# Kernel optimization log

Hardware: AMD Instinct MI355X
Metric: run time of the kernel (lower is better)

## Reference

```python
import jax, jax.numpy as jnp
import numpy as np

K = 16          # number of nearest neighbors (init kwarg k)
EPS = 1e-3      # denom threshold from the original code


def setup_inputs() -> dict:
    key = jax.random.key(0)
    k1, k2, k3 = jax.random.split(key, 3)
    V, F = 5000, 10000
    vertices = jax.random.normal(k1, (V, 3), dtype=jnp.float32)
    faces = jax.random.randint(k2, (F, 3), 0, V)
    probabilities = jax.random.uniform(k3, (F,), dtype=jnp.float32)
    return {"vertices": vertices, "faces": faces, "probabilities": probabilities}


def reference(vertices, faces, probabilities):
    F = faces.shape[0]
    pos = vertices[faces]                       # [F,3,3] triangle vertex coords
    bary = pos.mean(axis=1)                     # [F,3] barycenters

    # brute-force kNN over barycenters (x == y, so self is included like torch_geometric knn)
    sq = jnp.sum(bary * bary, axis=-1)          # [F]
    d2 = sq[:, None] + sq[None, :] - 2.0 * (bary @ bary.T)   # [F,F]
    _, nbr = jax.lax.top_k(-d2, K)              # [F,K] neighbor face indices

    # face normals
    e1 = pos[:, 1] - pos[:, 0]
    e2 = pos[:, 2] - pos[:, 0]
    n = jnp.cross(e1, e2)
    n = n / jnp.maximum(jnp.linalg.norm(n, axis=-1, keepdims=True), 1e-12)  # [F,3]

    # per (tri, neighbor, triangle-edge) plane intersection test
    nb_pos = pos[nbr]                           # [F,K,3,3] neighbor triangle vertices
    l0 = nb_pos                                 # segment starts
    l1 = jnp.roll(nb_pos, -1, axis=2)           # segment ends (k -> (k+1)%3)
    n_b = n[:, None, None, :]                   # [F,1,1,3]
    p0_b = pos[:, 0][:, None, None, :]          # [F,1,1,3] plane point of tri

    denom = jnp.sum(n_b * (l1 - l0), axis=-1)   # [F,K,3]
    numer = jnp.sum(n_b * (p0_b - l0), axis=-1) # [F,K,3]
    safe_denom = jnp.where(jnp.abs(denom) < EPS, 1.0, denom)
    t = numer / safe_denom
    hit = (jnp.abs(denom) >= EPS) & (t > 0.0) & (t < 1.0)   # [F,K,3]

    # early break in original => at most 1 increment per (tri, neighbor) pair
    pen = jnp.any(hit, axis=-1) & (nbr != jnp.arange(F)[:, None])  # [F,K]

    # scatter-add penetrations into neighbor_idx
    faces_penetrated = jnp.zeros((F,), jnp.float32).at[nbr.ravel()].add(
        pen.ravel().astype(jnp.float32))

    return jnp.dot(probabilities, faces_penetrated) / F
```

## Files before the change

kernel.cpp:

```cpp
#include <hip/hip_runtime.h>
#include <math.h>

#define KNN 16
#define EPS_F 0.001f
#define BLK 256

#define REP16(M) M(0) M(1) M(2) M(3) M(4) M(5) M(6) M(7) \
                 M(8) M(9) M(10) M(11) M(12) M(13) M(14) M(15)

#define CEAI(p,a,b) { int _lo = min(p##a, p##b); int _hi = max(p##a, p##b); p##a = _lo; p##b = _hi; }
#define CEDI(p,a,b) { int _lo = min(p##a, p##b); int _hi = max(p##a, p##b); p##a = _hi; p##b = _lo; }

#define SORT16I(p) \
  CEAI(p,0,1) CEDI(p,2,3) CEAI(p,4,5) CEDI(p,6,7) CEAI(p,8,9) CEDI(p,10,11) CEAI(p,12,13) CEDI(p,14,15) \
  CEAI(p,0,2) CEAI(p,1,3) CEDI(p,4,6) CEDI(p,5,7) CEAI(p,8,10) CEAI(p,9,11) CEDI(p,12,14) CEDI(p,13,15) \
  CEAI(p,0,1) CEAI(p,2,3) CEDI(p,4,5) CEDI(p,6,7) CEAI(p,8,9) CEAI(p,10,11) CEDI(p,12,13) CEDI(p,14,15) \
  CEAI(p,0,4) CEAI(p,1,5) CEAI(p,2,6) CEAI(p,3,7) CEDI(p,8,12) CEDI(p,9,13) CEDI(p,10,14) CEDI(p,11,15) \
  CEAI(p,0,2) CEAI(p,1,3) CEAI(p,4,6) CEAI(p,5,7) CEDI(p,8,10) CEDI(p,9,11) CEDI(p,12,14) CEDI(p,13,15) \
  CEAI(p,0,1) CEAI(p,2,3) CEAI(p,4,5) CEAI(p,6,7) CEDI(p,8,9) CEDI(p,10,11) CEDI(p,12,13) CEDI(p,14,15) \
  CEAI(p,0,8) CEAI(p,1,9) CEAI(p,2,10) CEAI(p,3,11) CEAI(p,4,12) CEAI(p,5,13) CEAI(p,6,14) CEAI(p,7,15) \
  CEAI(p,0,4) CEAI(p,1,5) CEAI(p,2,6) CEAI(p,3,7) CEAI(p,8,12) CEAI(p,9,13) CEAI(p,10,14) CEAI(p,11,15) \
  CEAI(p,0,2) CEAI(p,1,3) CEAI(p,4,6) CEAI(p,5,7) CEAI(p,8,10) CEAI(p,9,11) CEAI(p,12,14) CEAI(p,13,15) \
  CEAI(p,0,1) CEAI(p,2,3) CEAI(p,4,5) CEAI(p,6,7) CEAI(p,8,9) CEAI(p,10,11) CEAI(p,12,13) CEAI(p,14,15)

#define RESORT16I(p) \
  CEAI(p,0,8) CEAI(p,1,9) CEAI(p,2,10) CEAI(p,3,11) CEAI(p,4,12) CEAI(p,5,13) CEAI(p,6,14) CEAI(p,7,15) \
  CEAI(p,0,4) CEAI(p,1,5) CEAI(p,2,6) CEAI(p,3,7) CEAI(p,8,12) CEAI(p,9,13) CEAI(p,10,14) CEAI(p,11,15) \
  CEAI(p,0,2) CEAI(p,1,3) CEAI(p,4,6) CEAI(p,5,7) CEAI(p,8,10) CEAI(p,9,11) CEAI(p,12,14) CEAI(p,13,15) \
  CEAI(p,0,1) CEAI(p,2,3) CEAI(p,4,5) CEAI(p,6,7) CEAI(p,8,9) CEAI(p,10,11) CEAI(p,12,13) CEAI(p,14,15)

#define MERGE16I(r,x) \
  r##0=min(r##0,x##15); r##1=min(r##1,x##14); r##2=min(r##2,x##13); r##3=min(r##3,x##12); \
  r##4=min(r##4,x##11); r##5=min(r##5,x##10); r##6=min(r##6,x##9);  r##7=min(r##7,x##8);  \
  r##8=min(r##8,x##7);  r##9=min(r##9,x##6);  r##10=min(r##10,x##5); r##11=min(r##11,x##4); \
  r##12=min(r##12,x##3); r##13=min(r##13,x##2); r##14=min(r##14,x##1); r##15=min(r##15,x##0); \
  RESORT16I(r)

__device__ __forceinline__ float dist2(float4 q, float4 p) {
    return (q.w + p.w) - 2.0f * (q.x*p.x + q.y*p.y + q.z*p.z);
}

__device__ __forceinline__ int packkey(float d2, int j) {
    return (__float_as_int(d2) & 0xFFFFC000) | j;
}

__global__ __launch_bounds__(BLK) void prep_kernel(
    const float* __restrict__ verts, const int* __restrict__ faces,
    float4* __restrict__ baryq, float* __restrict__ nrm,
    float* __restrict__ p0s, int F)
{
    int f = blockIdx.x * BLK + threadIdx.x;
    if (f >= F) return;
    int i0 = faces[3*f+0], i1 = faces[3*f+1], i2 = faces[3*f+2];
    float ax = verts[3*i0+0], ay = verts[3*i0+1], az = verts[3*i0+2];
    float bx = verts[3*i1+0], by = verts[3*i1+1], bz = verts[3*i1+2];
    float cx = verts[3*i2+0], cy = verts[3*i2+1], cz = verts[3*i2+2];
    float gx = (ax + bx + cx) / 3.0f;
    float gy = (ay + by + cy) / 3.0f;
    float gz = (az + bz + cz) / 3.0f;
    float sq = gx*gx + gy*gy + gz*gz;
    baryq[f] = make_float4(gx, gy, gz, sq);
    float e1x = bx-ax, e1y = by-ay, e1z = bz-az;
    float e2x = cx-ax, e2y = cy-ay, e2z = cz-az;
    float nx = e1y*e2z - e1z*e2y;
    float ny = e1z*e2x - e1x*e2z;
    float nz = e1x*e2y - e1y*e2x;
    float len = sqrtf(nx*nx + ny*ny + nz*nz);
    float dn = fmaxf(len, 1e-12f);
    nrm[3*f+0] = nx/dn; nrm[3*f+1] = ny/dn; nrm[3*f+2] = nz/dn;
    p0s[3*f+0] = ax; p0s[3*f+1] = ay; p0s[3*f+2] = az;
}

__global__ __launch_bounds__(BLK) void knn_keys(
    const float4* __restrict__ baryq, int* __restrict__ cand_k,
    int F, int chunkLen)
{
    __shared__ float4 sb[BLK];
    int tid = threadIdx.x;
    int qi = blockIdx.x * BLK + tid;
    int qc = min(qi, F-1);
    float4 q = baryq[qc];
    #define DECLR(m) int r##m = 0x7fffffff;
    REP16(DECLR)
    #undef DECLR
    int jb = blockIdx.y * chunkLen;
    int je = min(jb + chunkLen, F);
    for (int base = jb; base < je; base += BLK) {
        int j = base + tid;
        sb[tid] = (j < je) ? baryq[j] : make_float4(0.f, 0.f, 0.f, INFINITY);
        __syncthreads();
        #pragma unroll 1
        for (int g = 0; g < BLK; g += 16) {
            #define MKKEY(m) int x##m = packkey(dist2(q, sb[g+(m)]), base+g+(m));
            REP16(MKKEY)
            #undef MKKEY
            SORT16I(x)
            MERGE16I(r, x)
        }
        __syncthreads();
    }
    if (qi < F) {
        size_t cb = (size_t)blockIdx.y * KNN * F + qi;
        #define STR(m) cand_k[cb + (size_t)(m) * F] = r##m;
        REP16(STR)
        #undef STR
    }
}

__global__ __launch_bounds__(BLK) void merge_nbr(
    const int* __restrict__ cand_k, int* __restrict__ nbr, int F, int nchunk)
{
    int qi = blockIdx.x * BLK + threadIdx.x;
    if (qi >= F) return;
    #define LDR(m) int r##m = cand_k[(size_t)(m) * F + qi];
    REP16(LDR)
    #undef LDR
    for (int c = 1; c < nchunk; ++c) {
        size_t cb = (size_t)c * KNN * F + qi;
        #define LDX(m) int x##m = cand_k[cb + (size_t)(m) * F];
        REP16(LDX)
        #undef LDX
        MERGE16I(r, x)
    }
    size_t ob = (size_t)qi * KNN;
    #define STN(m) nbr[ob + (m)] = r##m & 0x3FFF;
    REP16(STN)
    #undef STN
}

__device__ __forceinline__ bool edge_test(
    float nx, float ny, float nz, float px, float py, float pz,
    float ax, float ay, float az, float bx, float by, float bz)
{
    float denom = nx*(bx-ax) + ny*(by-ay) + nz*(bz-az);
    if (fabsf(denom) < EPS_F) return false;
    float numer = nx*(px-ax) + ny*(py-ay) + nz*(pz-az);
    float t = numer / denom;
    return (t > 0.0f) && (t < 1.0f);
}

__global__ __launch_bounds__(BLK) void pen_kernel(
    const float* __restrict__ verts, const int* __restrict__ faces,
    const float* __restrict__ prob, const int* __restrict__ nbr,
    const float* __restrict__ nrm, const float* __restrict__ p0s,
    float* __restrict__ partial, int F)
{
    int t = blockIdx.x * BLK + threadIdx.x;
    float val = 0.0f;
    int total = F * KNN;
    if (t < total) {
        int i = t >> 4;
        int j = nbr[t];
        if (j != i) {
            float nx = nrm[3*i+0], ny = nrm[3*i+1], nz = nrm[3*i+2];
            float px = p0s[3*i+0], py = p0s[3*i+1], pz = p0s[3*i+2];
            int j0 = faces[3*j+0], j1 = faces[3*j+1], j2 = faces[3*j+2];
            float ax = verts[3*j0+0], ay = verts[3*j0+1], az = verts[3*j0+2];
            float bx = verts[3*j1+0], by = verts[3*j1+1], bz = verts[3*j1+2];
            float cx = verts[3*j2+0], cy = verts[3*j2+1], cz = verts[3*j2+2];
            bool hit = edge_test(nx,ny,nz, px,py,pz, ax,ay,az, bx,by,bz)
                    || edge_test(nx,ny,nz, px,py,pz, bx,by,bz, cx,cy,cz)
                    || edge_test(nx,ny,nz, px,py,pz, cx,cy,cz, ax,ay,az);
            if (hit) val = prob[j];
        }
    }
    __shared__ float red[BLK];
    red[threadIdx.x] = val;
    __syncthreads();
    #pragma unroll
    for (int s = BLK/2; s > 0; s >>= 1) {
        if (threadIdx.x < s) red[threadIdx.x] += red[threadIdx.x + s];
        __syncthreads();
    }
    if (threadIdx.x == 0) partial[blockIdx.x] = red[0];
}

__global__ __launch_bounds__(BLK) void final_reduce(
    const float* __restrict__ partial, int n, float* __restrict__ out, int F)
{
    __shared__ float red[BLK];
    float s = 0.0f;
    for (int i = threadIdx.x; i < n; i += BLK) s += partial[i];
    red[threadIdx.x] = s;
    __syncthreads();
    #pragma unroll
    for (int st = BLK/2; st > 0; st >>= 1) {
        if (threadIdx.x < st) red[threadIdx.x] += red[threadIdx.x + st];
        __syncthreads();
    }
    if (threadIdx.x == 0) out[0] = red[0] / (float)F;
}

extern "C" void kernel_launch(void* const* d_in, const int* in_sizes, int n_in,
                              void* d_out, int out_size, void* d_ws, size_t ws_size,
                              hipStream_t stream)
{
    const float* verts = (const float*)d_in[0];
    const int*   faces = (const int*)d_in[1];
    const float* prob  = (const float*)d_in[2];
    float* out = (float*)d_out;
    int F = in_sizes[2];

    size_t off = 0;
    auto carve = [&](size_t bytes) {
        size_t cur = off;
        off += (bytes + 255) & ~(size_t)255;
        return cur;
    };
    char* w = (char*)d_ws;
    int nPenBlocks = (F * KNN + BLK - 1) / BLK;
    float4* baryq  = (float4*)(w + carve((size_t)F * sizeof(float4)));
    float*  nrm    = (float*)(w + carve((size_t)F * 3 * sizeof(float)));
    float*  p0s    = (float*)(w + carve((size_t)F * 3 * sizeof(float)));
    int*    nbr    = (int*)(w + carve((size_t)F * KNN * sizeof(int)));
    float*  partial= (float*)(w + carve((size_t)nPenBlocks * sizeof(float)));

    size_t perChunk = (size_t)F * KNN * sizeof(int) + 512;
    size_t remain = (ws_size > off) ? (ws_size - off) : 0;
    int nchunk = (int)(remain / perChunk);
    if (nchunk > 40) nchunk = 40;
    if (nchunk < 1) nchunk = 1;
    int chunkLen = (F + nchunk - 1) / nchunk;
    chunkLen = ((chunkLen + BLK - 1) / BLK) * BLK;
    nchunk = (F + chunkLen - 1) / chunkLen;
    int* cand_k = (int*)(w + carve((size_t)F * KNN * nchunk * sizeof(int)));

    int qBlocks = (F + BLK - 1) / BLK;

    prep_kernel<<<qBlocks, BLK, 0, stream>>>(verts, faces, baryq, nrm, p0s, F);
    knn_keys<<<dim3(qBlocks, nchunk), BLK, 0, stream>>>(baryq, cand_k, F, chunkLen);
    merge_nbr<<<qBlocks, BLK, 0, stream>>>(cand_k, nbr, F, nchunk);
    pen_kernel<<<nPenBlocks, BLK, 0, stream>>>(
        verts, faces, prob, nbr, nrm, p0s, partial, F);
    final_reduce<<<1, BLK, 0, stream>>>(partial, nPenBlocks, out, F);
}
```

Measured before the change: 96.36 us.

## Process two queries per thread in kNN and split candidate merge into two stages

The kNN kernel now runs 128-thread blocks where each thread keeps two query points and two top-16 lists. Each shared-memory candidate load is reused for both queries, and the inner loop is bounded by the valid chunk length so chunks can be 16-aligned instead of 256-aligned. The serial merge over up to 40 chunks becomes a two-level merge: groups of 8 chunks are merged in parallel across a 2D grid, then the groups are merged in a final pass. The goal is less shared-memory traffic per distance, finer chunk splitting, and more parallel merging. The cost is roughly double the register use per thread, which can lower occupancy, plus an extra kernel launch and intermediate buffer.

```diff
diff --git a/kernel.cpp b/kernel.cpp
--- a/kernel.cpp
+++ b/kernel.cpp
@@ -4,6 +4,7 @@
 #define KNN 16
 #define EPS_F 0.001f
 #define BLK 256
+#define BLKK 128
 
 #define REP16(M) M(0) M(1) M(2) M(3) M(4) M(5) M(6) M(7) \
                  M(8) M(9) M(10) M(11) M(12) M(13) M(14) M(15)
@@ -71,53 +72,87 @@
     p0s[3*f+0] = ax; p0s[3*f+1] = ay; p0s[3*f+2] = az;
 }
 
-__global__ __launch_bounds__(BLK) void knn_keys(
+__global__ __launch_bounds__(BLKK) void knn_keys(
     const float4* __restrict__ baryq, int* __restrict__ cand_k,
     int F, int chunkLen)
 {
-    __shared__ float4 sb[BLK];
+    __shared__ float4 sb[BLKK];
     int tid = threadIdx.x;
-    int qi = blockIdx.x * BLK + tid;
-    int qc = min(qi, F-1);
-    float4 q = baryq[qc];
-    #define DECLR(m) int r##m = 0x7fffffff;
-    REP16(DECLR)
-    #undef DECLR
+    int qa = blockIdx.x * (2*BLKK) + tid;
+    int qb = qa + BLKK;
+    float4 qA = baryq[min(qa, F-1)];
+    float4 qB = baryq[min(qb, F-1)];
+    #define DECLAB(m) int a##m = 0x7fffffff; int b##m = 0x7fffffff;
+    REP16(DECLAB)
+    #undef DECLAB
     int jb = blockIdx.y * chunkLen;
     int je = min(jb + chunkLen, F);
-    for (int base = jb; base < je; base += BLK) {
+    for (int base = jb; base < je; base += BLKK) {
         int j = base + tid;
         sb[tid] = (j < je) ? baryq[j] : make_float4(0.f, 0.f, 0.f, INFINITY);
         __syncthreads();
+        int lim = min(BLKK, je - base);
         #pragma unroll 1
-        for (int g = 0; g < BLK; g += 16) {
-            #define MKKEY(m) int x##m = packkey(dist2(q, sb[g+(m)]), base+g+(m));
-            REP16(MKKEY)
-            #undef MKKEY
-            SORT16I(x)
-            MERGE16I(r, x)
+        for (int g = 0; g < lim; g += 16) {
+            #define MKK(m) int xA##m, xB##m; { float4 P = sb[g+(m)]; \
+                int cj = base + g + (m); \
+                xA##m = packkey(dist2(qA, P), cj); \
+                xB##m = packkey(dist2(qB, P), cj); }
+            REP16(MKK)
+            #undef MKK
+            SORT16I(xA) SORT16I(xB)
+            MERGE16I(a, xA) MERGE16I(b, xB)
         }
         __syncthreads();
     }
-    if (qi < F) {
-        size_t cb = (size_t)blockIdx.y * KNN * F + qi;
-        #define STR(m) cand_k[cb + (size_t)(m) * F] = r##m;
-        REP16(STR)
-        #undef STR
-    }
-}
-
-__global__ __launch_bounds__(BLK) void merge_nbr(
-    const int* __restrict__ cand_k, int* __restrict__ nbr, int F, int nchunk)
+    size_t cb = (size_t)blockIdx.y * KNN * F;
+    if (qa < F) {
+        #define STA(m) cand_k[cb + (size_t)(m) * F + qa] = a##m;
+        REP16(STA)
+        #undef STA
+    }
+    if (qb < F) {
+        #define STB(m) cand_k[cb + (size_t)(m) * F + qb] = b##m;
+        REP16(STB)
+        #undef STB
+    }
+}
+
+__global__ __launch_bounds__(BLK) void merge_stage1(
+    const int* __restrict__ cand_k, int* __restrict__ cand2, int F, int nchunk)
 {
     int qi = blockIdx.x * BLK + threadIdx.x;
     if (qi >= F) return;
-    #define LDR(m) int r##m = cand_k[(size_t)(m) * F + qi];
+    int g = blockIdx.y;
+    int c0 = g * 8, c1 = min(c0 + 8, nchunk);
+    size_t b0 = (size_t)c0 * KNN * F + qi;
+    #define LDR(m) int r##m = cand_k[b0 + (size_t)(m) * F];
     REP16(LDR)
     #undef LDR
-    for (int c = 1; c < nchunk; ++c) {
+    for (int c = c0 + 1; c < c1; ++c) {
         size_t cb = (size_t)c * KNN * F + qi;
         #define LDX(m) int x##m = cand_k[cb + (size_t)(m) * F];
+        REP16(LDX)
+        #undef LDX
+        MERGE16I(r, x)
+    }
+    size_t ob = (size_t)g * KNN * F + qi;
+    #define STR(m) cand2[ob + (size_t)(m) * F] = r##m;
+    REP16(STR)
+    #undef STR
+}
+
+__global__ __launch_bounds__(BLK) void merge_stage2(
+    const int* __restrict__ cand2, int* __restrict__ nbr, int F, int ngroup)
+{
+    int qi = blockIdx.x * BLK + threadIdx.x;
+    if (qi >= F) return;
+    #define LDR(m) int r##m = cand2[(size_t)(m) * F + qi];
+    REP16(LDR)
+    #undef LDR
+    for (int c = 1; c < ngroup; ++c) {
+        size_t cb = (size_t)c * KNN * F + qi;
+        #define LDX(m) int x##m = cand2[cb + (size_t)(m) * F];
         REP16(LDX)
         #undef LDX
         MERGE16I(r, x)
@@ -208,28 +243,34 @@
         return cur;
     };
     char* w = (char*)d_ws;
+    const int NCHUNK_CAP = 40;
+    const int GMAX = (NCHUNK_CAP + 7) / 8;
     int nPenBlocks = (F * KNN + BLK - 1) / BLK;
     float4* baryq  = (float4*)(w + carve((size_t)F * sizeof(float4)));
     float*  nrm    = (float*)(w + carve((size_t)F * 3 * sizeof(float)));
     float*  p0s    = (float*)(w + carve((size_t)F * 3 * sizeof(float)));
     int*    nbr    = (int*)(w + carve((size_t)F * KNN * sizeof(int)));
     float*  partial= (float*)(w + carve((size_t)nPenBlocks * sizeof(float)));
+    int*    cand2  = (int*)(w + carve((size_t)GMAX * KNN * F * sizeof(int)));
 
     size_t perChunk = (size_t)F * KNN * sizeof(int) + 512;
     size_t remain = (ws_size > off) ? (ws_size - off) : 0;
     int nchunk = (int)(remain / perChunk);
-    if (nchunk > 40) nchunk = 40;
+    if (nchunk > NCHUNK_CAP) nchunk = NCHUNK_CAP;
     if (nchunk < 1) nchunk = 1;
     int chunkLen = (F + nchunk - 1) / nchunk;
-    chunkLen = ((chunkLen + BLK - 1) / BLK) * BLK;
+    chunkLen = ((chunkLen + 15) / 16) * 16;
     nchunk = (F + chunkLen - 1) / chunkLen;
     int* cand_k = (int*)(w + carve((size_t)F * KNN * nchunk * sizeof(int)));
-
-    int qBlocks = (F + BLK - 1) / BLK;
+    int ngroup = (nchunk + 7) / 8;
+
+    int qBlocks  = (F + BLK - 1) / BLK;
+    int qBlocks2 = (F + 2*BLKK - 1) / (2*BLKK);
 
     prep_kernel<<<qBlocks, BLK, 0, stream>>>(verts, faces, baryq, nrm, p0s, F);
-    knn_keys<<<dim3(qBlocks, nchunk), BLK, 0, stream>>>(baryq, cand_k, F, chunkLen);
-    merge_nbr<<<qBlocks, BLK, 0, stream>>>(cand_k, nbr, F, nchunk);
+    knn_keys<<<dim3(qBlocks2, nchunk), BLKK, 0, stream>>>(baryq, cand_k, F, chunkLen);
+    merge_stage1<<<dim3(qBlocks, ngroup), BLK, 0, stream>>>(cand_k, cand2, F, nchunk);
+    merge_stage2<<<qBlocks, BLK, 0, stream>>>(cand2, nbr, F, ngroup);
     pen_kernel<<<nPenBlocks, BLK, 0, stream>>>(
         verts, faces, prob, nbr, nrm, p0s, partial, F);
     final_reduce<<<1, BLK, 0, stream>>>(partial, nPenBlocks, out, F);
```

Result: no change. 97.63 us (+1.3%).

## Replace full kNN sort-merge with sampled threshold filter and candidate collection

Applied to the files above, without the earlier changes.

Exact kNN over all face pairs now runs in stages. First the 16th-nearest distance among a strided subsample of barycenters is computed per query and used as a threshold. Then a full pass only filters candidates at or under that threshold into per-query buffers, and a final sort selects the top 16. This removes the per-element bitonic sort and merge from the O(F^2) loop and also folds the -2 factor into precomputed coordinates so each distance is fused-multiply-adds. The cost is extra kernels and atomics. Correctness now depends on candidate counts fitting the per-chunk local cap of 21 and the global buffer cap, so overflow can silently drop true neighbours.

```diff
diff --git a/kernel.cpp b/kernel.cpp
--- a/kernel.cpp
+++ b/kernel.cpp
@@ -4,6 +4,9 @@
 #define KNN 16
 #define EPS_F 0.001f
 #define BLK 256
+#define LCAP 21
+#define SCH 16
+#define SSTRIDE 8
 
 #define REP16(M) M(0) M(1) M(2) M(3) M(4) M(5) M(6) M(7) \
                  M(8) M(9) M(10) M(11) M(12) M(13) M(14) M(15)
@@ -36,18 +39,17 @@
   r##12=min(r##12,x##3); r##13=min(r##13,x##2); r##14=min(r##14,x##1); r##15=min(r##15,x##0); \
   RESORT16I(r)
 
-__device__ __forceinline__ float dist2(float4 q, float4 p) {
-    return (q.w + p.w) - 2.0f * (q.x*p.x + q.y*p.y + q.z*p.z);
-}
-
+__device__ __forceinline__ float distf(float4 q, float4 P) {
+    return fmaf(q.x, P.x, fmaf(q.y, P.y, fmaf(q.z, P.z, q.w + P.w)));
+}
 __device__ __forceinline__ int packkey(float d2, int j) {
     return (__float_as_int(d2) & 0xFFFFC000) | j;
 }
 
 __global__ __launch_bounds__(BLK) void prep_kernel(
     const float* __restrict__ verts, const int* __restrict__ faces,
-    float4* __restrict__ baryq, float* __restrict__ nrm,
-    float* __restrict__ p0s, int F)
+    float4* __restrict__ baryq, float4* __restrict__ baryqm,
+    float* __restrict__ nrm, float* __restrict__ p0s, int F)
 {
     int f = blockIdx.x * BLK + threadIdx.x;
     if (f >= F) return;
@@ -59,7 +61,8 @@
     float gy = (ay + by + cy) / 3.0f;
     float gz = (az + bz + cz) / 3.0f;
     float sq = gx*gx + gy*gy + gz*gz;
-    baryq[f] = make_float4(gx, gy, gz, sq);
+    baryq[f]  = make_float4(gx, gy, gz, sq);
+    baryqm[f] = make_float4(-2.0f*gx, -2.0f*gy, -2.0f*gz, sq);
     float e1x = bx-ax, e1y = by-ay, e1z = bz-az;
     float e2x = cx-ax, e2y = cy-ay, e2z = cz-az;
     float nx = e1y*e2z - e1z*e2y;
@@ -71,55 +74,119 @@
     p0s[3*f+0] = ax; p0s[3*f+1] = ay; p0s[3*f+2] = az;
 }
 
-__global__ __launch_bounds__(BLK) void knn_keys(
-    const float4* __restrict__ baryq, int* __restrict__ cand_k,
-    int F, int chunkLen)
+__global__ __launch_bounds__(BLK) void knn_sample(
+    const float4* __restrict__ baryq, const float4* __restrict__ baryqm,
+    int* __restrict__ samp_k, int F, int SLEN)
 {
     __shared__ float4 sb[BLK];
     int tid = threadIdx.x;
     int qi = blockIdx.x * BLK + tid;
-    int qc = min(qi, F-1);
-    float4 q = baryq[qc];
+    float4 q = baryq[min(qi, F-1)];
     #define DECLR(m) int r##m = 0x7fffffff;
     REP16(DECLR)
     #undef DECLR
-    int jb = blockIdx.y * chunkLen;
-    int je = min(jb + chunkLen, F);
+    int sbase = blockIdx.y * SLEN;
+    if (tid < SLEN) {
+        int j = (sbase + tid) * SSTRIDE;
+        sb[tid] = (j < F) ? baryqm[j] : make_float4(0.f, 0.f, 0.f, INFINITY);
+    }
+    __syncthreads();
+    #pragma unroll 1
+    for (int g = 0; g < SLEN; g += 16) {
+        #define MKK(m) int x##m = packkey(distf(q, sb[g+(m)]), (sbase+g+(m))*SSTRIDE);
+        REP16(MKK)
+        #undef MKK
+        SORT16I(x)
+        MERGE16I(r, x)
+    }
+    if (qi < F) {
+        size_t cb = (size_t)blockIdx.y * KNN * F + qi;
+        #define STR(m) samp_k[cb + (size_t)(m) * F] = r##m;
+        REP16(STR)
+        #undef STR
+    }
+}
+
+__global__ __launch_bounds__(BLK) void merge_T(
+    const int* __restrict__ samp_k, int* __restrict__ Tkey,
+    int* __restrict__ cnt, int F)
+{
+    int qi = blockIdx.x * BLK + threadIdx.x;
+    if (qi >= F) return;
+    #define LDR(m) int r##m = samp_k[(size_t)(m) * F + qi];
+    REP16(LDR)
+    #undef LDR
+    for (int c = 1; c < SCH; ++c) {
+        size_t cb = (size_t)c * KNN * F + qi;
+        #define LDX(m) int x##m = samp_k[cb + (size_t)(m) * F];
+        REP16(LDX)
+        #undef LDX
+        MERGE16I(r, x)
+    }
+    Tkey[qi] = r15;
+    cnt[qi] = 0;
+}
+
+__global__ __launch_bounds__(BLK) void collect_kernel(
+    const float4* __restrict__ baryq, const float4* __restrict__ baryqm,
+    const int* __restrict__ Tkey, int* __restrict__ cnt,
+    int* __restrict__ buf, int F, int CLEN, int CAP)
+{
+    __shared__ float4 sb[BLK];
+    __shared__ int lb[BLK * LCAP];
+    int tid = threadIdx.x;
+    int qi = blockIdx.x * BLK + tid;
+    bool active = qi < F;
+    int qc = min(qi, F-1);
+    float4 q = baryq[qc];
+    int T = Tkey[qc];
+    int lcnt = 0;
+    int jb = blockIdx.y * CLEN;
+    int je = min(jb + CLEN, F);
     for (int base = jb; base < je; base += BLK) {
         int j = base + tid;
-        sb[tid] = (j < je) ? baryq[j] : make_float4(0.f, 0.f, 0.f, INFINITY);
+        sb[tid] = (j < je) ? baryqm[j] : make_float4(0.f, 0.f, 0.f, INFINITY);
         __syncthreads();
+        int lim = (min(BLK, je - base) + 15) & ~15;
         #pragma unroll 1
-        for (int g = 0; g < BLK; g += 16) {
-            #define MKKEY(m) int x##m = packkey(dist2(q, sb[g+(m)]), base+g+(m));
-            REP16(MKKEY)
-            #undef MKKEY
-            SORT16I(x)
-            MERGE16I(r, x)
+        for (int g = 0; g < lim; g += 16) {
+            #define CSTEP(m) { float4 P = sb[g+(m)]; \
+                int key = packkey(distf(q, P), base + g + (m)); \
+                lb[tid * LCAP + min(lcnt, LCAP-1)] = key; \
+                lcnt += (active && key <= T) ? 1 : 0; }
+            REP16(CSTEP)
+            #undef CSTEP
         }
         __syncthreads();
     }
-    if (qi < F) {
-        size_t cb = (size_t)blockIdx.y * KNN * F + qi;
-        #define STR(m) cand_k[cb + (size_t)(m) * F] = r##m;
-        REP16(STR)
-        #undef STR
-    }
-}
-
-__global__ __launch_bounds__(BLK) void merge_nbr(
-    const int* __restrict__ cand_k, int* __restrict__ nbr, int F, int nchunk)
+    lcnt = min(lcnt, LCAP);
+    if (active && lcnt > 0) {
+        int basep = atomicAdd(&cnt[qi], lcnt);
+        for (int k = 0; k < lcnt; ++k) {
+            int p = basep + k;
+            if (p < CAP) buf[(size_t)qi * CAP + p] = lb[tid * LCAP + k];
+        }
+    }
+}
+
+__global__ __launch_bounds__(BLK) void final_select(
+    const int* __restrict__ buf, const int* __restrict__ cnt,
+    int* __restrict__ nbr, int F, int CAP)
 {
     int qi = blockIdx.x * BLK + threadIdx.x;
     if (qi >= F) return;
-    #define LDR(m) int r##m = cand_k[(size_t)(m) * F + qi];
-    REP16(LDR)
-    #undef LDR
-    for (int c = 1; c < nchunk; ++c) {
-        size_t cb = (size_t)c * KNN * F + qi;
-        #define LDX(m) int x##m = cand_k[cb + (size_t)(m) * F];
-        REP16(LDX)
-        #undef LDX
+    int n = min(cnt[qi], CAP);
+    const int* row = buf + (size_t)qi * CAP;
+    #define DECLR(m) int r##m = 0x7fffffff;
+    REP16(DECLR)
+    #undef DECLR
+    #pragma unroll 1
+    for (int t = 0; t < n; t += 16) {
+        #define LSEL(m) int x##m; { int v = row[t + (m)]; \
+            x##m = (t + (m) < n) ? v : 0x7fffffff; }
+        REP16(LSEL)
+        #undef LSEL
+        SORT16I(x)
         MERGE16I(r, x)
     }
     size_t ob = (size_t)qi * KNN;
@@ -210,26 +277,36 @@
     char* w = (char*)d_ws;
     int nPenBlocks = (F * KNN + BLK - 1) / BLK;
     float4* baryq  = (float4*)(w + carve((size_t)F * sizeof(float4)));
+    float4* baryqm = (float4*)(w + carve((size_t)F * sizeof(float4)));
     float*  nrm    = (float*)(w + carve((size_t)F * 3 * sizeof(float)));
     float*  p0s    = (float*)(w + carve((size_t)F * 3 * sizeof(float)));
     int*    nbr    = (int*)(w + carve((size_t)F * KNN * sizeof(int)));
     float*  partial= (float*)(w + carve((size_t)nPenBlocks * sizeof(float)));
-
-    size_t perChunk = (size_t)F * KNN * sizeof(int) + 512;
+    int*    Tkey   = (int*)(w + carve((size_t)F * sizeof(int)));
+    int*    cnt    = (int*)(w + carve((size_t)F * sizeof(int)));
+    int*    samp_k = (int*)(w + carve((size_t)SCH * KNN * F * sizeof(int)));
+
     size_t remain = (ws_size > off) ? (ws_size - off) : 0;
-    int nchunk = (int)(remain / perChunk);
-    if (nchunk > 40) nchunk = 40;
-    if (nchunk < 1) nchunk = 1;
-    int chunkLen = (F + nchunk - 1) / nchunk;
-    chunkLen = ((chunkLen + BLK - 1) / BLK) * BLK;
-    nchunk = (F + chunkLen - 1) / chunkLen;
-    int* cand_k = (int*)(w + carve((size_t)F * KNN * nchunk * sizeof(int)));
+    int CAP = (int)(remain / ((size_t)F * sizeof(int)));
+    if (CAP > 448) CAP = 448;
+    if (CAP < 320) CAP = 320;
+    CAP &= ~15;
+    int* buf = (int*)(w + carve((size_t)F * CAP * sizeof(int)));
+
+    int nSamp = (F + SSTRIDE - 1) / SSTRIDE;
+    int SLEN = ((nSamp + SCH - 1) / SCH + 15) & ~15;
+    int CCH = 40;
+    int CLEN = (((F + CCH - 1) / CCH + BLK - 1) / BLK) * BLK;
+    int nCChunk = (F + CLEN - 1) / CLEN;
 
     int qBlocks = (F + BLK - 1) / BLK;
 
-    prep_kernel<<<qBlocks, BLK, 0, stream>>>(verts, faces, baryq, nrm, p0s, F);
-    knn_keys<<<dim3(qBlocks, nchunk), BLK, 0, stream>>>(baryq, cand_k, F, chunkLen);
-    merge_nbr<<<qBlocks, BLK, 0, stream>>>(cand_k, nbr, F, nchunk);
+    prep_kernel<<<qBlocks, BLK, 0, stream>>>(verts, faces, baryq, baryqm, nrm, p0s, F);
+    knn_sample<<<dim3(qBlocks, SCH), BLK, 0, stream>>>(baryq, baryqm, samp_k, F, SLEN);
+    merge_T<<<qBlocks, BLK, 0, stream>>>(samp_k, Tkey, cnt, F);
+    collect_kernel<<<dim3(qBlocks, nCChunk), BLK, 0, stream>>>(
+        baryq, baryqm, Tkey, cnt, buf, F, CLEN, CAP);
+    final_select<<<qBlocks, BLK, 0, stream>>>(buf, cnt, nbr, F, CAP);
     pen_kernel<<<nPenBlocks, BLK, 0, stream>>>(
         verts, faces, prob, nbr, nrm, p0s, partial, F);
     final_reduce<<<1, BLK, 0, stream>>>(partial, nPenBlocks, out, F);
```

New measurement: 94.36 us. -2.1%, faster.
